# Performance work log

Hardware: AMD Instinct MI355X
Metric: run time of the kernel (lower is better)

The kernel has to match this reference:

```python
import jax, jax.numpy as jnp
import numpy as np

R = 16
ALPHA = 32
SCALING = ALPHA / R  # 2.0


def setup_inputs() -> dict:
    key = jax.random.key(0)
    k1, k2, k3, k4, k5 = jax.random.split(key, 5)
    x = jax.random.normal(k1, (8192, 4096), dtype=jnp.float32)
    W = jax.random.normal(k2, (4096, 4096), dtype=jnp.float32) * 0.02
    b = jax.random.normal(k3, (4096,), dtype=jnp.float32) * 0.02
    A = jax.random.uniform(k4, (R, 4096), dtype=jnp.float32)
    B = jax.random.normal(k5, (4096, R), dtype=jnp.float32) * 0.02
    return {"x": x, "W": W, "b": b, "A": A, "B": B}


def reference(x, W, b, A, B):
    # base linear: x @ W.T + b
    base = jnp.einsum("ni,oi->no", x, W) + b
    # LoRA path, reassociated: scaling * ((x @ A.T) @ B.T)
    # mathematically identical to x @ (scaling * (B @ A)).T but O(r*(in+out)) per token
    lora = SCALING * jnp.einsum("nr,or->no", jnp.einsum("ni,ri->nr", x, A), B)
    return base + lora
```

## Files before the change

kernel.cpp:

```cpp
#include <hip/hip_runtime.h>
#include <stdint.h>

typedef unsigned short u16;
typedef __bf16 bf16x8 __attribute__((ext_vector_type(8)));
typedef u16   u16x8  __attribute__((ext_vector_type(8)));
typedef float f32x4  __attribute__((ext_vector_type(4)));

#define GLOBAL_AS __attribute__((address_space(1)))
#define LDS_AS __attribute__((address_space(3)))

#define MDIM 8192
#define NDIM 4096
#define KDIM 4096
#define RDIM 16

#define BM 128
#define BN 128
#define BK 64
#define EXTS 40

#define XBF_OFF 0
#define WBF_OFF (MDIM * KDIM * 2)
#define ABF_OFF (WBF_OFF + NDIM * KDIM * 2)
#define T_OFF   (ABF_OFF + RDIM * KDIM * 2)
#define WS_NEED ((size_t)T_OFF + MDIM * RDIM * 4)

#define XN8 (MDIM * KDIM / 8)
#define WN8 (NDIM * KDIM / 8)
#define AN8 (RDIM * KDIM / 8)

__device__ __forceinline__ u16 f2bf(float f) {
    union { float f; uint32_t u; } un;
    un.f = f;
    uint32_t u = un.u;
    u += 0x7FFFu + ((u >> 16) & 1u);
    return (u16)(u >> 16);
}

__device__ __forceinline__ void cvt8(const float* __restrict__ p, u16* __restrict__ d) {
    f32x4 a = *(const f32x4*)p;
    f32x4 b = *(const f32x4*)(p + 4);
    u16x8 o;
    o[0] = f2bf(a[0]); o[1] = f2bf(a[1]); o[2] = f2bf(a[2]); o[3] = f2bf(a[3]);
    o[4] = f2bf(b[0]); o[5] = f2bf(b[1]); o[6] = f2bf(b[2]); o[7] = f2bf(b[3]);
    *(u16x8*)d = o;
}

__global__ __launch_bounds__(256) void cvt_all_kernel(
        const float* __restrict__ x, const float* __restrict__ W,
        const float* __restrict__ A,
        u16* __restrict__ xbf, u16* __restrict__ Wbf, u16* __restrict__ Abf) {
    const int total = XN8 + WN8 + AN8;
    int i = blockIdx.x * blockDim.x + threadIdx.x;
    const int stride = gridDim.x * blockDim.x;
    for (; i < total; i += stride) {
        if (i < XN8) {
            cvt8(x + (size_t)i * 8, xbf + (size_t)i * 8);
        } else if (i < XN8 + WN8) {
            const int j = i - XN8;
            cvt8(W + (size_t)j * 8, Wbf + (size_t)j * 8);
        } else {
            const int j = i - XN8 - WN8;
            cvt8(A + (size_t)j * 8, Abf + (size_t)j * 8);
        }
    }
}

__global__ __launch_bounds__(256) void lora_t_kernel(
        const u16* __restrict__ x, const u16* __restrict__ A,
        float* __restrict__ t) {
    const int wave = threadIdx.x >> 6;
    const int lane = threadIdx.x & 63;
    const int rl   = lane & 15;
    const int quad = lane >> 4;
    const int m0   = (blockIdx.x * 4 + wave) * 16;

    const u16* xp = x + (size_t)(m0 + rl) * KDIM + quad * 8;
    const u16* ap = A + (size_t)rl * KDIM + quad * 8;

    f32x4 acc = {0.f, 0.f, 0.f, 0.f};
#pragma unroll 8
    for (int k = 0; k < KDIM; k += 32) {
        bf16x8 av = *(const bf16x8*)(xp + k);
        bf16x8 bv = *(const bf16x8*)(ap + k);
        acc = __builtin_amdgcn_mfma_f32_16x16x32_bf16(av, bv, acc, 0, 0, 0);
    }
    const int orow = m0 + quad * 4;
#pragma unroll
    for (int v = 0; v < 4; ++v)
        t[(size_t)(orow + v) * RDIM + rl] = acc[v];
}

__global__ __launch_bounds__(256) void lora_t_inline_kernel(
        const float* __restrict__ x, const float* __restrict__ A,
        float* __restrict__ t) {
    const int wave = threadIdx.x >> 6;
    const int lane = threadIdx.x & 63;
    const int rl   = lane & 15;
    const int quad = lane >> 4;
    const int m0   = (blockIdx.x * 4 + wave) * 16;

    const float* xp = x + (size_t)(m0 + rl) * KDIM + quad * 8;
    const float* ap = A + (size_t)rl * KDIM + quad * 8;

    f32x4 acc = {0.f, 0.f, 0.f, 0.f};
    for (int k = 0; k < KDIM; k += 32) {
        f32x4 a0 = *(const f32x4*)(xp + k), a1 = *(const f32x4*)(xp + k + 4);
        f32x4 b0 = *(const f32x4*)(ap + k), b1 = *(const f32x4*)(ap + k + 4);
        u16x8 av, bv;
#pragma unroll
        for (int j = 0; j < 4; ++j) {
            av[j] = f2bf(a0[j]); av[j + 4] = f2bf(a1[j]);
            bv[j] = f2bf(b0[j]); bv[j + 4] = f2bf(b1[j]);
        }
        acc = __builtin_amdgcn_mfma_f32_16x16x32_bf16(
            (bf16x8)av, (bf16x8)bv, acc, 0, 0, 0);
    }
    const int orow = m0 + quad * 4;
#pragma unroll
    for (int v = 0; v < 4; ++v)
        t[(size_t)(orow + v) * RDIM + rl] = acc[v];
}

#define BK2   64
#define HTILE 8192
#define ABUF  16384
#define BOFFS 32768
#define NKT   (KDIM / BK2)

#define STAGE(gsrc, half, kt, par, ab) do {                                   \
    const int _b = (par) * ABUF + (ab) * BOFFS + (half) * HTILE;              \
    _Pragma("unroll")                                                         \
    for (int _q = 0; _q < 2; ++_q) {                                          \
        const int _c   = _q * 512 + tid;                                      \
        const int _row = _c >> 3;                                             \
        const int _kc  = (_c & 7) ^ (_row & 7);                               \
        __builtin_amdgcn_global_load_lds(                                     \
            (const GLOBAL_AS uint32_t*)((gsrc) +                              \
                (size_t)((half) * 128 + _row) * KDIM + (kt) * BK2 + _kc * 8), \
            (LDS_AS uint32_t*)(smem + _b + _c * 8), 16, 0, 0);                \
    } } while (0)

#define NOSTAGE ((void)0)
#define VM4 asm volatile("s_waitcnt vmcnt(4)" ::: "memory")
#define VM0 asm volatile("s_waitcnt vmcnt(0)" ::: "memory")
#define LGKM0 asm volatile("s_waitcnt lgkmcnt(0)" ::: "memory")

#define READ_A(dst, abase) do {                                               \
    _Pragma("unroll")                                                         \
    for (int i = 0; i < 4; ++i) {                                             \
        const int r_ = wm * 64 + i * 16 + rl;                                 \
        _Pragma("unroll")                                                     \
        for (int kk = 0; kk < 2; ++kk)                                        \
            dst[i][kk] = *(const bf16x8*)((abase) + r_ * 64 +                 \
                                          (((kk * 4 + q4) ^ (r_ & 7)) * 8));  \
    } } while (0)

#define READ_B(dst, bbase) do {                                               \
    _Pragma("unroll")                                                         \
    for (int j = 0; j < 2; ++j) {                                             \
        const int r_ = wn * 32 + j * 16 + rl;                                 \
        _Pragma("unroll")                                                     \
        for (int kk = 0; kk < 2; ++kk)                                        \
            dst[j][kk] = *(const bf16x8*)((bbase) + r_ * 64 +                 \
                                          (((kk * 4 + q4) ^ (r_ & 7)) * 8));  \
    } } while (0)

#define MFMA_Q(QM, QN, a_, b_) do {                                           \
    __builtin_amdgcn_s_setprio(1);                                            \
    _Pragma("unroll")                                                         \
    for (int i = 0; i < 4; ++i)                                               \
        _Pragma("unroll")                                                     \
        for (int j = 0; j < 2; ++j)                                           \
            _Pragma("unroll")                                                 \
            for (int kk = 0; kk < 2; ++kk)                                    \
                acc[QM][QN][i][j] = __builtin_amdgcn_mfma_f32_16x16x32_bf16(  \
                    a_[i][kk], b_[j][kk], acc[QM][QN][i][j], 0, 0, 0);        \
    __builtin_amdgcn_s_setprio(0);                                            \
} while (0)

#define BARRIER __builtin_amdgcn_s_barrier()

#define KTILE(BC, S1, S2, S3, S4, W4) do {                                    \
    bf16x8 a_[4][2], b0_[2][2], b1_[2][2];                                    \
    const u16* _ab = smem + (BC) * ABUF;                                      \
    const u16* _bb = smem + BOFFS + (BC) * ABUF;                              \
                                                      \
    READ_A(a_, _ab);                                                          \
    READ_B(b0_, _bb);                                                         \
    S1; BARRIER; LGKM0; MFMA_Q(0, 0, a_, b0_); BARRIER;                       \
                                               \
    READ_B(b1_, _bb + HTILE);                                                 \
    S2; BARRIER; LGKM0; MFMA_Q(0, 1, a_, b1_); BARRIER;                       \
                                               \
    READ_A(a_, _ab + HTILE);                                                  \
    S3; BARRIER; LGKM0; MFMA_Q(1, 0, a_, b0_); BARRIER;                       \
                                      \
    S4; BARRIER; MFMA_Q(1, 1, a_, b1_); W4; BARRIER;                          \
} while (0)

__global__ __launch_bounds__(512, 2) void gemm8_lora_kernel(
        const u16* __restrict__ x, const u16* __restrict__ W,
        const float* __restrict__ bias, const float* __restrict__ Bl,
        const float* __restrict__ tmat, float* __restrict__ out) {
    __shared__ __align__(16) u16 smem[65536];

    const int tid  = threadIdx.x;
    const int lane = tid & 63;
    const int wave = tid >> 6;
    const int wm   = wave >> 2;
    const int wn   = wave & 3;
    const int rl   = lane & 15;
    const int q4   = lane >> 4;
    const int bm   = blockIdx.y * 256;
    const int bn   = blockIdx.x * 256;

    const u16* gA = x + (size_t)bm * KDIM;
    const u16* gB = W + (size_t)bn * KDIM;

    f32x4 acc[2][2][4][2];
#pragma unroll
    for (int a = 0; a < 2; ++a)
#pragma unroll
        for (int b = 0; b < 2; ++b)
#pragma unroll
            for (int i = 0; i < 4; ++i)
#pragma unroll
                for (int j = 0; j < 2; ++j)
                    acc[a][b][i][j] = (f32x4){0.f, 0.f, 0.f, 0.f};

    STAGE(gA, 0, 0, 0, 0); STAGE(gB, 0, 0, 0, 1);
    STAGE(gA, 1, 0, 0, 0); STAGE(gB, 1, 0, 0, 1);
    STAGE(gA, 0, 1, 1, 0); STAGE(gB, 0, 1, 1, 1);
    VM4;
    BARRIER;

    for (int t = 0; t < NKT - 2; t += 2) {
        KTILE(0, STAGE(gA, 1, t + 1, 1, 0), STAGE(gB, 1, t + 1, 1, 1),
                 STAGE(gA, 0, t + 2, 0, 0), STAGE(gB, 0, t + 2, 0, 1), VM4);
        KTILE(1, STAGE(gA, 1, t + 2, 0, 0), STAGE(gB, 1, t + 2, 0, 1),
                 STAGE(gA, 0, t + 3, 1, 0), STAGE(gB, 0, t + 3, 1, 1), VM4);
    }

    KTILE(0, STAGE(gA, 1, NKT - 1, 1, 0), STAGE(gB, 1, NKT - 1, 1, 1),
             NOSTAGE, NOSTAGE, VM0);
    KTILE(1, NOSTAGE, NOSTAGE, NOSTAGE, NOSTAGE, NOSTAGE);

    {
        u16x8 z = {0, 0, 0, 0, 0, 0, 0, 0};
        if (tid < 256) {
            const float* tp = tmat + (size_t)(bm + tid) * RDIM;
            u16* d = smem + tid * 32;
            f32x4 t0 = *(const f32x4*)tp,       t1 = *(const f32x4*)(tp + 4);
            f32x4 t2 = *(const f32x4*)(tp + 8), t3 = *(const f32x4*)(tp + 12);
            u16x8 o0, o1;
#pragma unroll
            for (int j = 0; j < 4; ++j) {
                o0[j] = f2bf(2.0f * t0[j]); o0[j + 4] = f2bf(2.0f * t1[j]);
                o1[j] = f2bf(2.0f * t2[j]); o1[j + 4] = f2bf(2.0f * t3[j]);
            }
            *(u16x8*)d = o0; *(u16x8*)(d + 8) = o1;
            *(u16x8*)(d + 16) = z; *(u16x8*)(d + 24) = z;
        } else {
            const int r = tid - 256;
            const float* bp = Bl + (size_t)(bn + r) * RDIM;
            u16* d = smem + BOFFS + r * 32;
            f32x4 b0 = *(const f32x4*)bp,       b1 = *(const f32x4*)(bp + 4);
            f32x4 b2 = *(const f32x4*)(bp + 8), b3 = *(const f32x4*)(bp + 12);
            u16x8 o0, o1;
#pragma unroll
            for (int j = 0; j < 4; ++j) {
                o0[j] = f2bf(b0[j]); o0[j + 4] = f2bf(b1[j]);
                o1[j] = f2bf(b2[j]); o1[j + 4] = f2bf(b3[j]);
            }
            *(u16x8*)d = o0; *(u16x8*)(d + 8) = o1;
            *(u16x8*)(d + 16) = z; *(u16x8*)(d + 24) = z;
        }
    }
    __syncthreads();

    {
        bf16x8 ae[2][4], be[2][2];
#pragma unroll
        for (int h = 0; h < 2; ++h)
#pragma unroll
            for (int i = 0; i < 4; ++i) {
                const int r_ = h * 128 + wm * 64 + i * 16 + rl;
                ae[h][i] = *(const bf16x8*)(smem + r_ * 32 + q4 * 8);
            }
#pragma unroll
        for (int h = 0; h < 2; ++h)
#pragma unroll
            for (int j = 0; j < 2; ++j) {
                const int r_ = h * 128 + wn * 32 + j * 16 + rl;
                be[h][j] = *(const bf16x8*)(smem + BOFFS + r_ * 32 + q4 * 8);
            }
#pragma unroll
        for (int a = 0; a < 2; ++a)
#pragma unroll
            for (int b = 0; b < 2; ++b)
#pragma unroll
                for (int i = 0; i < 4; ++i)
#pragma unroll
                    for (int j = 0; j < 2; ++j)
                        acc[a][b][i][j] = __builtin_amdgcn_mfma_f32_16x16x32_bf16(
                            ae[a][i], be[b][j], acc[a][b][i][j], 0, 0, 0);
    }

    float bv[2][2];
#pragma unroll
    for (int h = 0; h < 2; ++h)
#pragma unroll
        for (int j = 0; j < 2; ++j)
            bv[h][j] = bias[bn + h * 128 + wn * 32 + j * 16 + rl];
#pragma unroll
    for (int a = 0; a < 2; ++a)
#pragma unroll
        for (int i = 0; i < 4; ++i) {
            const int row0 = bm + a * 128 + wm * 64 + i * 16 + q4 * 4;
#pragma unroll
            for (int b = 0; b < 2; ++b)
#pragma unroll
                for (int j = 0; j < 2; ++j) {
                    const int gcol = bn + b * 128 + wn * 32 + j * 16 + rl;
#pragma unroll
                    for (int v = 0; v < 4; ++v)
                        out[(size_t)(row0 + v) * NDIM + gcol] =
                            acc[a][b][i][j][v] + bv[b][j];
                }
        }
}

__device__ __forceinline__ void stage_ext_b(
        int tid, int bm, int bn,
        const float* __restrict__ t, const float* __restrict__ bias,
        const float* __restrict__ Bl, u16* eA, u16* eB) {
    if (tid < 128) {
        const int r = tid;
        const float* tp = t + (size_t)(bm + r) * RDIM;
        u16* d = eA + r * EXTS;
#pragma unroll
        for (int j = 0; j < RDIM; ++j) d[j] = f2bf(2.0f * tp[j]);
        d[16] = 0x3F80;
#pragma unroll
        for (int j = 17; j < 32; ++j) d[j] = 0;
    } else {
        const int r = tid - 128;
        const float* bp = Bl + (size_t)(bn + r) * RDIM;
        u16* d = eB + r * EXTS;
#pragma unroll
        for (int j = 0; j < RDIM; ++j) d[j] = f2bf(bp[j]);
        d[16] = f2bf(bias[bn + r]);
#pragma unroll
        for (int j = 17; j < 32; ++j) d[j] = 0;
    }
}

__global__ __launch_bounds__(256) void gemm_lora_inline_kernel(
        const float* __restrict__ x, const float* __restrict__ W,
        const float* __restrict__ bias, const float* __restrict__ Bl,
        const float* __restrict__ t, float* __restrict__ out) {
    __shared__ __align__(16) u16 sA[BM * BK];
    __shared__ __align__(16) u16 sB[BN * BK];
    __shared__ __align__(16) u16 sAe[BM * EXTS];
    __shared__ __align__(16) u16 sBe[BN * EXTS];

    const int tid  = threadIdx.x;
    const int lane = tid & 63;
    const int wave = tid >> 6;
    const int wm   = wave >> 1;
    const int wn   = wave & 1;
    const int rl   = lane & 15;
    const int quad = lane >> 4;
    const int bm   = blockIdx.y * BM;
    const int bn   = blockIdx.x * BN;

    stage_ext_b(tid, bm, bn, t, bias, Bl, sAe, sBe);

    const float* gA = x + (size_t)bm * KDIM;
    const float* gB = W + (size_t)bn * KDIM;

    const int row0 = tid >> 3;
    const int kc0  = tid & 7;

    f32x4 acc[4][4];
#pragma unroll
    for (int i = 0; i < 4; ++i)
#pragma unroll
        for (int j = 0; j < 4; ++j)
            acc[i][j] = (f32x4){0.f, 0.f, 0.f, 0.f};

    for (int kt = 0; kt < KDIM; kt += BK) {
        u16x8 ra[4], rb[4];
#pragma unroll
        for (int q = 0; q < 4; ++q) {
            const int row = q * 32 + row0;
            const int kc  = kc0 ^ (row & 7);
            const size_t base = (size_t)row * KDIM + kt + kc * 8;
            f32x4 a0 = *(const f32x4*)(gA + base), a1 = *(const f32x4*)(gA + base + 4);
            f32x4 b0 = *(const f32x4*)(gB + base), b1 = *(const f32x4*)(gB + base + 4);
#pragma unroll
            for (int j = 0; j < 4; ++j) {
                ra[q][j] = f2bf(a0[j]); ra[q][j + 4] = f2bf(a1[j]);
                rb[q][j] = f2bf(b0[j]); rb[q][j + 4] = f2bf(b1[j]);
            }
        }
        __syncthreads();
#pragma unroll
        for (int q = 0; q < 4; ++q) {
            const int c = q * 256 + tid;
            *(u16x8*)(sA + c * 8) = ra[q];
            *(u16x8*)(sB + c * 8) = rb[q];
        }
        __syncthreads();

#pragma unroll
        for (int kk = 0; kk < 2; ++kk) {
            const int lc = kk * 4 + quad;
            bf16x8 af[4], bfv[4];
#pragma unroll
            for (int i = 0; i < 4; ++i) {
                const int rra = wm * 64 + i * 16 + rl;
                const int rrb = wn * 64 + i * 16 + rl;
                af[i]  = *(const bf16x8*)(sA + rra * BK + (lc ^ (rra & 7)) * 8);
                bfv[i] = *(const bf16x8*)(sB + rrb * BK + (lc ^ (rrb & 7)) * 8);
            }
#pragma unroll
            for (int i = 0; i < 4; ++i)
#pragma unroll
                for (int j = 0; j < 4; ++j)
                    acc[i][j] = __builtin_amdgcn_mfma_f32_16x16x32_bf16(
                        af[i], bfv[j], acc[i][j], 0, 0, 0);
        }
    }

    {
        const int ko = quad * 8;
        bf16x8 af[4], bfv[4];
#pragma unroll
        for (int i = 0; i < 4; ++i) {
            af[i]  = *(const bf16x8*)(sAe + (wm * 64 + i * 16 + rl) * EXTS + ko);
            bfv[i] = *(const bf16x8*)(sBe + (wn * 64 + i * 16 + rl) * EXTS + ko);
        }
#pragma unroll
        for (int i = 0; i < 4; ++i)
#pragma unroll
            for (int j = 0; j < 4; ++j)
                acc[i][j] = __builtin_amdgcn_mfma_f32_16x16x32_bf16(
                    af[i], bfv[j], acc[i][j], 0, 0, 0);
    }

#pragma unroll
    for (int i = 0; i < 4; ++i) {
        const int grow = bm + wm * 64 + i * 16 + quad * 4;
#pragma unroll
        for (int j = 0; j < 4; ++j) {
            const int gcol = bn + wn * 64 + j * 16 + rl;
#pragma unroll
            for (int v = 0; v < 4; ++v)
                out[(size_t)(grow + v) * NDIM + gcol] = acc[i][j][v];
        }
    }
}

extern "C" void kernel_launch(void* const* d_in, const int* in_sizes, int n_in,
                              void* d_out, int out_size, void* d_ws, size_t ws_size,
                              hipStream_t stream) {
    const float* x  = (const float*)d_in[0];
    const float* W  = (const float*)d_in[1];
    const float* b  = (const float*)d_in[2];
    const float* A  = (const float*)d_in[3];
    const float* Bl = (const float*)d_in[4];
    float* out = (float*)d_out;
    char* ws = (char*)d_ws;

    if (ws_size >= WS_NEED) {
        u16*   xbf = (u16*)(ws + XBF_OFF);
        u16*   Wbf = (u16*)(ws + WBF_OFF);
        u16*   Abf = (u16*)(ws + ABF_OFF);
        float* t   = (float*)(ws + T_OFF);

        dim3 grid8(NDIM / 256, MDIM / 256);
        cvt_all_kernel<<<4096, 256, 0, stream>>>(x, W, A, xbf, Wbf, Abf);
        lora_t_kernel<<<128, 256, 0, stream>>>(xbf, Abf, t);
        gemm8_lora_kernel<<<grid8, 512, 0, stream>>>(xbf, Wbf, b, Bl, t, out);
    } else {
        float* t = (float*)ws;
        dim3 grid(NDIM / BN, MDIM / BM);
        lora_t_inline_kernel<<<128, 256, 0, stream>>>(x, A, t);
        gemm_lora_inline_kernel<<<grid, 256, 0, stream>>>(x, W, b, Bl, t, out);
    }
}
```

Measured before the change: 531.6 us.

## Software-pipeline LDS fragment reads across k-tiles and cut barriers per tile

Restructures the main GEMM k-loop so LDS fragment reads for the next quadrant or next k-tile are issued before the MFMAs that use the current fragments. Register double-buffering (a0f/a1f, b0f/b1f) replaces the explicit lgkmcnt waits. Barriers per k-tile drop from eight to two, meant to reduce sync stalls and overlap LDS latency with MFMA work. It raises register pressure under launch_bounds(512,2) and depends on the vmcnt waits and barrier placement being correct for the shared-buffer reuse.

```diff
diff --git a/kernel.cpp b/kernel.cpp
--- a/kernel.cpp
+++ b/kernel.cpp
@@ -144,7 +144,6 @@
 #define NOSTAGE ((void)0)
 #define VM4 asm volatile("s_waitcnt vmcnt(4)" ::: "memory")
 #define VM0 asm volatile("s_waitcnt vmcnt(0)" ::: "memory")
-#define LGKM0 asm volatile("s_waitcnt lgkmcnt(0)" ::: "memory")
 
 #define READ_A(dst, abase) do {                                               \
     _Pragma("unroll")                                                         \
@@ -181,22 +180,29 @@
 
 #define BARRIER __builtin_amdgcn_s_barrier()
 
-#define KTILE(BC, S1, S2, S3, S4, W4) do {                                    \
-    bf16x8 a_[4][2], b0_[2][2], b1_[2][2];                                    \
-    const u16* _ab = smem + (BC) * ABUF;                                      \
-    const u16* _bb = smem + BOFFS + (BC) * ABUF;                              \
-                                                      \
-    READ_A(a_, _ab);                                                          \
-    READ_B(b0_, _bb);                                                         \
-    S1; BARRIER; LGKM0; MFMA_Q(0, 0, a_, b0_); BARRIER;                       \
-                                               \
-    READ_B(b1_, _bb + HTILE);                                                 \
-    S2; BARRIER; LGKM0; MFMA_Q(0, 1, a_, b1_); BARRIER;                       \
-                                               \
-    READ_A(a_, _ab + HTILE);                                                  \
-    S3; BARRIER; LGKM0; MFMA_Q(1, 0, a_, b0_); BARRIER;                       \
-                                      \
-    S4; BARRIER; MFMA_Q(1, 1, a_, b1_); W4; BARRIER;                          \
+#define KT(BC, S1, S2, S3, S4, RD34, W2, W4) do {                             \
+    const u16* _ab  = smem + (BC) * ABUF;                                     \
+    const u16* _bb  = smem + BOFFS + (BC) * ABUF;                             \
+    const u16* _abN = smem + ((BC) ^ 1) * ABUF;                               \
+    const u16* _bbN = smem + BOFFS + ((BC) ^ 1) * ABUF;                       \
+                                                                      \
+    READ_B(b1f, _bb + HTILE);                                                 \
+    S1;                                                                       \
+    MFMA_Q(0, 0, a0f, b0f);                                                   \
+                                                                      \
+    READ_A(a1f, _ab + HTILE);                                                 \
+    S2;                                                                       \
+    MFMA_Q(0, 1, a0f, b1f);                                                   \
+    W2; BARRIER;                                                              \
+                                                                      \
+    if (RD34) READ_A(a0f, _abN);                                              \
+    S3;                                                                       \
+    MFMA_Q(1, 1, a1f, b1f);                                                   \
+                         \
+    MFMA_Q(1, 0, a1f, b0f);                                                   \
+    if (RD34) READ_B(b0f, _bbN);                                              \
+    S4;                                                                       \
+    W4; BARRIER;                                                              \
 } while (0)
 
 __global__ __launch_bounds__(512, 2) void gemm8_lora_kernel(
@@ -229,22 +235,27 @@
                 for (int j = 0; j < 2; ++j)
                     acc[a][b][i][j] = (f32x4){0.f, 0.f, 0.f, 0.f};
 
+    bf16x8 a0f[4][2], a1f[4][2], b0f[2][2], b1f[2][2];
+
     STAGE(gA, 0, 0, 0, 0); STAGE(gB, 0, 0, 0, 1);
     STAGE(gA, 1, 0, 0, 0); STAGE(gB, 1, 0, 0, 1);
     STAGE(gA, 0, 1, 1, 0); STAGE(gB, 0, 1, 1, 1);
     VM4;
     BARRIER;
+    READ_A(a0f, smem);
+    READ_B(b0f, smem + BOFFS);
 
     for (int t = 0; t < NKT - 2; t += 2) {
-        KTILE(0, STAGE(gA, 1, t + 1, 1, 0), STAGE(gB, 1, t + 1, 1, 1),
-                 STAGE(gA, 0, t + 2, 0, 0), STAGE(gB, 0, t + 2, 0, 1), VM4);
-        KTILE(1, STAGE(gA, 1, t + 2, 0, 0), STAGE(gB, 1, t + 2, 0, 1),
-                 STAGE(gA, 0, t + 3, 1, 0), STAGE(gB, 0, t + 3, 1, 1), VM4);
-    }
-
-    KTILE(0, STAGE(gA, 1, NKT - 1, 1, 0), STAGE(gB, 1, NKT - 1, 1, 1),
-             NOSTAGE, NOSTAGE, VM0);
-    KTILE(1, NOSTAGE, NOSTAGE, NOSTAGE, NOSTAGE, NOSTAGE);
+        KT(0, STAGE(gA, 1, t + 1, 1, 0), STAGE(gB, 1, t + 1, 1, 1),
+              STAGE(gA, 0, t + 2, 0, 0), STAGE(gB, 0, t + 2, 0, 1),
+              1, VM4, VM4);
+        KT(1, STAGE(gA, 1, t + 2, 0, 0), STAGE(gB, 1, t + 2, 0, 1),
+              STAGE(gA, 0, t + 3, 1, 0), STAGE(gB, 0, t + 3, 1, 1),
+              1, VM4, VM4);
+    }
+    KT(0, STAGE(gA, 1, NKT - 1, 1, 0), STAGE(gB, 1, NKT - 1, 1, 1),
+          NOSTAGE, NOSTAGE, 1, VM4, VM0);
+    KT(1, NOSTAGE, NOSTAGE, NOSTAGE, NOSTAGE, 0, NOSTAGE, NOSTAGE);
 
     {
         u16x8 z = {0, 0, 0, 0, 0, 0, 0, 0};
```

Measured after the change: 698.2 us. 1.31x slower.

## Switch main GEMM to 32x32x16 MFMA with register double-buffered LDS reads

Applied to the files above, without the earlier changes.

Replaces the 16x16x32 MFMA tiling with 32x32x16 MFMA tiles, which need fewer LDS fragment reads per flop. Fragment reads are double-buffered in registers so the next k-slice loads while the current MFMAs run. The per-quadrant barriers and waitcnts are dropped in favour of one barrier per k-tile. The global prefetch becomes a simple two-buffer scheme that waits with vmcnt(0) each tile, which may expose more global memory latency than the earlier deeper staging. The LoRA epilogue is compacted to a 16-wide layout to match the new MFMA shape.

```diff
diff --git a/kernel.cpp b/kernel.cpp
--- a/kernel.cpp
+++ b/kernel.cpp
@@ -5,6 +5,7 @@
 typedef __bf16 bf16x8 __attribute__((ext_vector_type(8)));
 typedef u16   u16x8  __attribute__((ext_vector_type(8)));
 typedef float f32x4  __attribute__((ext_vector_type(4)));
+typedef float f32x16 __attribute__((ext_vector_type(16)));
 
 #define GLOBAL_AS __attribute__((address_space(1)))
 #define LDS_AS __attribute__((address_space(3)))
@@ -142,61 +143,54 @@
     } } while (0)
 
 #define NOSTAGE ((void)0)
-#define VM4 asm volatile("s_waitcnt vmcnt(4)" ::: "memory")
 #define VM0 asm volatile("s_waitcnt vmcnt(0)" ::: "memory")
-#define LGKM0 asm volatile("s_waitcnt lgkmcnt(0)" ::: "memory")
-
-#define READ_A(dst, abase) do {                                               \
+
+#define READ_A32(dst, ab_, c) do {                                            \
     _Pragma("unroll")                                                         \
-    for (int i = 0; i < 4; ++i) {                                             \
-        const int r_ = wm * 64 + i * 16 + rl;                                 \
+    for (int h = 0; h < 2; ++h)                                               \
         _Pragma("unroll")                                                     \
-        for (int kk = 0; kk < 2; ++kk)                                        \
-            dst[i][kk] = *(const bf16x8*)((abase) + r_ * 64 +                 \
-                                          (((kk * 4 + q4) ^ (r_ & 7)) * 8));  \
+        for (int r = 0; r < 2; ++r) {                                         \
+            const int rh = wm * 64 + r * 32 + l31;                            \
+            dst[h][r] = *(const bf16x8*)((ab_) + h * HTILE + rh * 64 +        \
+                                         ((((c) * 2 + hi) ^ (rh & 7)) * 8));  \
+        } } while (0)
+
+#define READ_B32(dst, bb_, c) do {                                            \
+    _Pragma("unroll")                                                         \
+    for (int cb = 0; cb < 2; ++cb) {                                          \
+        const int rh = wn * 32 + l31;                                         \
+        dst[cb] = *(const bf16x8*)((bb_) + cb * HTILE + rh * 64 +             \
+                                   ((((c) * 2 + hi) ^ (rh & 7)) * 8));        \
     } } while (0)
 
-#define READ_B(dst, bbase) do {                                               \
-    _Pragma("unroll")                                                         \
-    for (int j = 0; j < 2; ++j) {                                             \
-        const int r_ = wn * 32 + j * 16 + rl;                                 \
-        _Pragma("unroll")                                                     \
-        for (int kk = 0; kk < 2; ++kk)                                        \
-            dst[j][kk] = *(const bf16x8*)((bbase) + r_ * 64 +                 \
-                                          (((kk * 4 + q4) ^ (r_ & 7)) * 8));  \
-    } } while (0)
-
-#define MFMA_Q(QM, QN, a_, b_) do {                                           \
+#define MFMA32(a_, b_) do {                                                   \
     __builtin_amdgcn_s_setprio(1);                                            \
     _Pragma("unroll")                                                         \
-    for (int i = 0; i < 4; ++i)                                               \
+    for (int h = 0; h < 2; ++h)                                               \
         _Pragma("unroll")                                                     \
-        for (int j = 0; j < 2; ++j)                                           \
+        for (int r = 0; r < 2; ++r)                                           \
             _Pragma("unroll")                                                 \
-            for (int kk = 0; kk < 2; ++kk)                                    \
-                acc[QM][QN][i][j] = __builtin_amdgcn_mfma_f32_16x16x32_bf16(  \
-                    a_[i][kk], b_[j][kk], acc[QM][QN][i][j], 0, 0, 0);        \
+            for (int cb = 0; cb < 2; ++cb)                                    \
+                acc[h][r][cb] = __builtin_amdgcn_mfma_f32_32x32x16_bf16(      \
+                    a_[h][r], b_[cb], acc[h][r][cb], 0, 0, 0);                \
     __builtin_amdgcn_s_setprio(0);                                            \
 } while (0)
 
 #define BARRIER __builtin_amdgcn_s_barrier()
 
-#define KTILE(BC, S1, S2, S3, S4, W4) do {                                    \
-    bf16x8 a_[4][2], b0_[2][2], b1_[2][2];                                    \
-    const u16* _ab = smem + (BC) * ABUF;                                      \
-    const u16* _bb = smem + BOFFS + (BC) * ABUF;                              \
-                                                      \
-    READ_A(a_, _ab);                                                          \
-    READ_B(b0_, _bb);                                                         \
-    S1; BARRIER; LGKM0; MFMA_Q(0, 0, a_, b0_); BARRIER;                       \
-                                               \
-    READ_B(b1_, _bb + HTILE);                                                 \
-    S2; BARRIER; LGKM0; MFMA_Q(0, 1, a_, b1_); BARRIER;                       \
-                                               \
-    READ_A(a_, _ab + HTILE);                                                  \
-    S3; BARRIER; LGKM0; MFMA_Q(1, 0, a_, b0_); BARRIER;                       \
-                                      \
-    S4; BARRIER; MFMA_Q(1, 1, a_, b1_); W4; BARRIER;                          \
+#define KT32(ab_, bb_, S1, S2, S3, S4, WEND) do {                             \
+    READ_A32(aF, ab_, 0); READ_B32(bF, bb_, 0);                               \
+    S1; S2;                                                                   \
+    READ_A32(aN, ab_, 1); READ_B32(bN, bb_, 1);                               \
+    MFMA32(aF, bF);                                                           \
+    S3;                                                                       \
+    READ_A32(aF, ab_, 2); READ_B32(bF, bb_, 2);                               \
+    MFMA32(aN, bN);                                                           \
+    S4;                                                                       \
+    READ_A32(aN, ab_, 3); READ_B32(bN, bb_, 3);                               \
+    MFMA32(aF, bF);                                                           \
+    MFMA32(aN, bN);                                                           \
+    WEND; BARRIER;                                                            \
 } while (0)
 
 __global__ __launch_bounds__(512, 2) void gemm8_lora_kernel(
@@ -210,124 +204,115 @@
     const int wave = tid >> 6;
     const int wm   = wave >> 2;
     const int wn   = wave & 3;
-    const int rl   = lane & 15;
-    const int q4   = lane >> 4;
+    const int l31  = lane & 31;
+    const int hi   = lane >> 5;
     const int bm   = blockIdx.y * 256;
     const int bn   = blockIdx.x * 256;
 
     const u16* gA = x + (size_t)bm * KDIM;
     const u16* gB = W + (size_t)bn * KDIM;
 
-    f32x4 acc[2][2][4][2];
-#pragma unroll
-    for (int a = 0; a < 2; ++a)
-#pragma unroll
-        for (int b = 0; b < 2; ++b)
-#pragma unroll
-            for (int i = 0; i < 4; ++i)
-#pragma unroll
-                for (int j = 0; j < 2; ++j)
-                    acc[a][b][i][j] = (f32x4){0.f, 0.f, 0.f, 0.f};
-
-    STAGE(gA, 0, 0, 0, 0); STAGE(gB, 0, 0, 0, 1);
-    STAGE(gA, 1, 0, 0, 0); STAGE(gB, 1, 0, 0, 1);
-    STAGE(gA, 0, 1, 1, 0); STAGE(gB, 0, 1, 1, 1);
-    VM4;
+    f32x16 acc[2][2][2];
+#pragma unroll
+    for (int h = 0; h < 2; ++h)
+#pragma unroll
+        for (int r = 0; r < 2; ++r)
+#pragma unroll
+            for (int cb = 0; cb < 2; ++cb)
+                acc[h][r][cb] = (f32x16)(0.f);
+
+    bf16x8 aF[2][2], aN[2][2], bF[2], bN[2];
+
+    STAGE(gA, 0, 0, 0, 0); STAGE(gA, 1, 0, 0, 0);
+    STAGE(gB, 0, 0, 0, 1); STAGE(gB, 1, 0, 0, 1);
+    VM0;
     BARRIER;
 
-    for (int t = 0; t < NKT - 2; t += 2) {
-        KTILE(0, STAGE(gA, 1, t + 1, 1, 0), STAGE(gB, 1, t + 1, 1, 1),
-                 STAGE(gA, 0, t + 2, 0, 0), STAGE(gB, 0, t + 2, 0, 1), VM4);
-        KTILE(1, STAGE(gA, 1, t + 2, 0, 0), STAGE(gB, 1, t + 2, 0, 1),
-                 STAGE(gA, 0, t + 3, 1, 0), STAGE(gB, 0, t + 3, 1, 1), VM4);
-    }
-
-    KTILE(0, STAGE(gA, 1, NKT - 1, 1, 0), STAGE(gB, 1, NKT - 1, 1, 1),
-             NOSTAGE, NOSTAGE, VM0);
-    KTILE(1, NOSTAGE, NOSTAGE, NOSTAGE, NOSTAGE, NOSTAGE);
-
+    for (int t = 0; t < NKT - 1; ++t) {
+        const u16* ab = smem + (t & 1) * ABUF;
+        const u16* bb = smem + BOFFS + (t & 1) * ABUF;
+        const int par = (t & 1) ^ 1;
+        KT32(ab, bb,
+             STAGE(gA, 0, t + 1, par, 0), STAGE(gA, 1, t + 1, par, 0),
+             STAGE(gB, 0, t + 1, par, 1), STAGE(gB, 1, t + 1, par, 1),
+             VM0);
+    }
     {
-        u16x8 z = {0, 0, 0, 0, 0, 0, 0, 0};
-        if (tid < 256) {
-            const float* tp = tmat + (size_t)(bm + tid) * RDIM;
-            u16* d = smem + tid * 32;
-            f32x4 t0 = *(const f32x4*)tp,       t1 = *(const f32x4*)(tp + 4);
-            f32x4 t2 = *(const f32x4*)(tp + 8), t3 = *(const f32x4*)(tp + 12);
-            u16x8 o0, o1;
-#pragma unroll
-            for (int j = 0; j < 4; ++j) {
-                o0[j] = f2bf(2.0f * t0[j]); o0[j + 4] = f2bf(2.0f * t1[j]);
-                o1[j] = f2bf(2.0f * t2[j]); o1[j + 4] = f2bf(2.0f * t3[j]);
+        const u16* ab = smem + ABUF;
+        const u16* bb = smem + BOFFS + ABUF;
+        KT32(ab, bb, NOSTAGE, NOSTAGE, NOSTAGE, NOSTAGE, NOSTAGE);
+    }
+
+    if (tid < 256) {
+        const float* tp = tmat + (size_t)(bm + tid) * RDIM;
+        u16* d = smem + tid * 16;
+        f32x4 t0 = *(const f32x4*)tp,       t1 = *(const f32x4*)(tp + 4);
+        f32x4 t2 = *(const f32x4*)(tp + 8), t3 = *(const f32x4*)(tp + 12);
+        u16x8 o0, o1;
+#pragma unroll
+        for (int j = 0; j < 4; ++j) {
+            o0[j] = f2bf(2.0f * t0[j]); o0[j + 4] = f2bf(2.0f * t1[j]);
+            o1[j] = f2bf(2.0f * t2[j]); o1[j + 4] = f2bf(2.0f * t3[j]);
+        }
+        *(u16x8*)d = o0; *(u16x8*)(d + 8) = o1;
+    } else {
+        const int r = tid - 256;
+        const float* bp = Bl + (size_t)(bn + r) * RDIM;
+        u16* d = smem + 4096 + r * 16;
+        f32x4 b0 = *(const f32x4*)bp,       b1 = *(const f32x4*)(bp + 4);
+        f32x4 b2 = *(const f32x4*)(bp + 8), b3 = *(const f32x4*)(bp + 12);
+        u16x8 o0, o1;
+#pragma unroll
+        for (int j = 0; j < 4; ++j) {
+            o0[j] = f2bf(b0[j]); o0[j + 4] = f2bf(b1[j]);
+            o1[j] = f2bf(b2[j]); o1[j + 4] = f2bf(b3[j]);
+        }
+        *(u16x8*)d = o0; *(u16x8*)(d + 8) = o1;
+    }
+    __syncthreads();
+
+    {
+        bf16x8 ae[2][2], be[2];
+#pragma unroll
+        for (int h = 0; h < 2; ++h)
+#pragma unroll
+            for (int r = 0; r < 2; ++r) {
+                const int row = h * 128 + wm * 64 + r * 32 + l31;
+                ae[h][r] = *(const bf16x8*)(smem + row * 16 + hi * 8);
             }
-            *(u16x8*)d = o0; *(u16x8*)(d + 8) = o1;
-            *(u16x8*)(d + 16) = z; *(u16x8*)(d + 24) = z;
-        } else {
-            const int r = tid - 256;
-            const float* bp = Bl + (size_t)(bn + r) * RDIM;
-            u16* d = smem + BOFFS + r * 32;
-            f32x4 b0 = *(const f32x4*)bp,       b1 = *(const f32x4*)(bp + 4);
-            f32x4 b2 = *(const f32x4*)(bp + 8), b3 = *(const f32x4*)(bp + 12);
-            u16x8 o0, o1;
-#pragma unroll
-            for (int j = 0; j < 4; ++j) {
-                o0[j] = f2bf(b0[j]); o0[j + 4] = f2bf(b1[j]);
-                o1[j] = f2bf(b2[j]); o1[j + 4] = f2bf(b3[j]);
+#pragma unroll
+        for (int cb = 0; cb < 2; ++cb) {
+            const int row = cb * 128 + wn * 32 + l31;
+            be[cb] = *(const bf16x8*)(smem + 4096 + row * 16 + hi * 8);
+        }
+#pragma unroll
+        for (int h = 0; h < 2; ++h)
+#pragma unroll
+            for (int r = 0; r < 2; ++r)
+#pragma unroll
+                for (int cb = 0; cb < 2; ++cb)
+                    acc[h][r][cb] = __builtin_amdgcn_mfma_f32_32x32x16_bf16(
+                        ae[h][r], be[cb], acc[h][r][cb], 0, 0, 0);
+    }
+
+    float bv[2];
+#pragma unroll
+    for (int cb = 0; cb < 2; ++cb)
+        bv[cb] = bias[bn + cb * 128 + wn * 32 + l31];
+#pragma unroll
+    for (int h = 0; h < 2; ++h)
+#pragma unroll
+        for (int r = 0; r < 2; ++r) {
+            const int row0 = bm + h * 128 + wm * 64 + r * 32 + 4 * hi;
+#pragma unroll
+            for (int cb = 0; cb < 2; ++cb) {
+                const int gcol = bn + cb * 128 + wn * 32 + l31;
+#pragma unroll
+                for (int reg = 0; reg < 16; ++reg) {
+                    const int grow = row0 + (reg & 3) + 8 * (reg >> 2);
+                    out[(size_t)grow * NDIM + gcol] = acc[h][r][cb][reg] + bv[cb];
+                }
             }
-            *(u16x8*)d = o0; *(u16x8*)(d + 8) = o1;
-            *(u16x8*)(d + 16) = z; *(u16x8*)(d + 24) = z;
-        }
-    }
-    __syncthreads();
-
-    {
-        bf16x8 ae[2][4], be[2][2];
-#pragma unroll
-        for (int h = 0; h < 2; ++h)
-#pragma unroll
-            for (int i = 0; i < 4; ++i) {
-                const int r_ = h * 128 + wm * 64 + i * 16 + rl;
-                ae[h][i] = *(const bf16x8*)(smem + r_ * 32 + q4 * 8);
-            }
-#pragma unroll
-        for (int h = 0; h < 2; ++h)
-#pragma unroll
-            for (int j = 0; j < 2; ++j) {
-                const int r_ = h * 128 + wn * 32 + j * 16 + rl;
-                be[h][j] = *(const bf16x8*)(smem + BOFFS + r_ * 32 + q4 * 8);
-            }
-#pragma unroll
-        for (int a = 0; a < 2; ++a)
-#pragma unroll
-            for (int b = 0; b < 2; ++b)
-#pragma unroll
-                for (int i = 0; i < 4; ++i)
-#pragma unroll
-                    for (int j = 0; j < 2; ++j)
-                        acc[a][b][i][j] = __builtin_amdgcn_mfma_f32_16x16x32_bf16(
-                            ae[a][i], be[b][j], acc[a][b][i][j], 0, 0, 0);
-    }
-
-    float bv[2][2];
-#pragma unroll
-    for (int h = 0; h < 2; ++h)
-#pragma unroll
-        for (int j = 0; j < 2; ++j)
-            bv[h][j] = bias[bn + h * 128 + wn * 32 + j * 16 + rl];
-#pragma unroll
-    for (int a = 0; a < 2; ++a)
-#pragma unroll
-        for (int i = 0; i < 4; ++i) {
-            const int row0 = bm + a * 128 + wm * 64 + i * 16 + q4 * 4;
-#pragma unroll
-            for (int b = 0; b < 2; ++b)
-#pragma unroll
-                for (int j = 0; j < 2; ++j) {
-                    const int gcol = bn + b * 128 + wn * 32 + j * 16 + rl;
-#pragma unroll
-                    for (int v = 0; v < 4; ++v)
-                        out[(size_t)(row0 + v) * NDIM + gcol] =
-                            acc[a][b][i][j][v] + bv[b][j];
-                }
         }
 }
 
```

Result: slower. 566.5 us (+6.6%).
